# Performance work log

Hardware: AMD Instinct MI355X
Metric: run time of the kernel (lower is better)

Reference implementation:

```python
import jax, jax.numpy as jnp
import numpy as np
from jax import lax

N_NODES = 50000
N_EDGES = 1_600_000
B, T = 4, 12
GCN_H, TCN_H, OUT_LEN = 32, 32, 1


def setup_inputs() -> dict:
    key = jax.random.key(0)
    ks = jax.random.split(key, 8)
    return {
        "x_seq": jax.random.normal(ks[0], (B, T, N_NODES), jnp.float32),
        "edge_index": jax.random.randint(ks[1], (2, N_EDGES), 0, N_NODES, jnp.int64),
        "edge_weight": jax.random.uniform(ks[2], (N_EDGES,), jnp.float32),
        "gcn_w": jax.random.normal(ks[3], (1, GCN_H), jnp.float32) * 0.5,
        "gcn_b": jnp.zeros((GCN_H,), jnp.float32),
        "conv_w": jax.random.normal(ks[4], (TCN_H, GCN_H, 3), jnp.float32) * 0.1,
        "conv_b": jnp.zeros((TCN_H,), jnp.float32),
        "lin_w": jax.random.normal(ks[5], (TCN_H, OUT_LEN), jnp.float32) * 0.1,
        "lin_b": jnp.zeros((OUT_LEN,), jnp.float32),
    }


def _gcn_agg(x, src, dst, norm, n):
    msgs = x[:, src] * norm[None, :]                      # [BT, E+N]
    return jax.vmap(lambda m: jax.ops.segment_sum(m, dst, num_segments=n))(msgs)


def reference(x_seq, edge_index, edge_weight, gcn_w, gcn_b, conv_w, conv_b, lin_w, lin_b):
    b, t, n = x_seq.shape
    src, dst = edge_index[0], edge_index[1]
    # GCN normalization with self-loops (fill_value=1.0), as PyG GCNConv
    loops = jnp.arange(n)
    src_f = jnp.concatenate([src, loops])
    dst_f = jnp.concatenate([dst, loops])
    ew_f = jnp.concatenate([edge_weight, jnp.ones((n,), x_seq.dtype)])
    deg = jax.ops.segment_sum(ew_f, dst_f, num_segments=n)
    dinv = jnp.where(deg > 0, deg ** -0.5, 0.0)
    norm = dinv[src_f] * ew_f * dinv[dst_f]               # [E+N]
    # GCN is linear: A_hat (X W) == (A_hat X) W ; X has 1 channel -> aggregate scalars
    x = x_seq.reshape(b * t, n)                           # [BT, N]
    agg = _gcn_agg(x, src_f, dst_f, norm, n)              # [BT, N]
    h = agg[..., None] * gcn_w[0][None, None, :] + gcn_b  # [BT, N, H]
    # temporal conv over T: reshape to [B*N, H, T]
    h = h.reshape(b, t, n, GCN_H).transpose(0, 2, 3, 1).reshape(b * n, GCN_H, t)
    y = lax.conv_general_dilated(h, conv_w, window_strides=(1,), padding=[(1, 1)],
                                 dimension_numbers=("NCH", "OIH", "NCH"))
    y = jax.nn.relu(y + conv_b[None, :, None])            # [B*N, H, T]
    pooled = y.mean(axis=-1)                              # [B*N, H]
    out = pooled @ lin_w + lin_b                          # [B*N, out_len]
    return out.reshape(b, n, -1).transpose(0, 2, 1)       # [B, out_len, N]
```

## Files before the change

kernel.cpp:

```cpp
#include <hip/hip_runtime.h>
#include <hip/hip_fp16.h>
#include <math.h>

#define N_NODES 50000
#define N_EDGES 1600000
#define BT 48
#define CAP 80
#define BINSZ 64
#define NBINS 782
#define ECHUNK 4096
#define SBLOCK 1024

__global__ __launch_bounds__(SBLOCK) void stage_k(const int* __restrict__ ei,
                                                  const float* __restrict__ ew,
                                                  int* __restrict__ stage_cnt,
                                                  int2* __restrict__ staged,
                                                  int scap) {
  __shared__ int hist[NBINS];
  __shared__ int ptr[NBINS];
  int t = threadIdx.x;
  for (int b = t; b < NBINS; b += SBLOCK) hist[b] = 0;
  __syncthreads();

  int e0 = blockIdx.x * ECHUNK;
  int ne = min(ECHUNK, N_EDGES - e0);

  for (int k = t; k < ne; k += SBLOCK) {
    int d = ei[N_EDGES + e0 + k];
    atomicAdd(&hist[d >> 6], 1);
  }
  __syncthreads();
  for (int b = t; b < NBINS; b += SBLOCK) {
    int h = hist[b];
    ptr[b] = h ? atomicAdd(&stage_cnt[b], h) : 0;
  }
  __syncthreads();
  for (int k = t; k < ne; k += SBLOCK) {
    int e = e0 + k;
    int s = ei[e];
    int d = ei[N_EDGES + e];
    float w = ew[e];
    int b = d >> 6;
    int p = atomicAdd(&ptr[b], 1);
    if (p < scap)
      staged[(size_t)b * scap + p] = make_int2(s | ((d & 63) << 16), __float_as_int(w));
  }
}

__global__ __launch_bounds__(256) void build_k(const int2* __restrict__ staged,
                                               const int* __restrict__ stage_cnt,
                                               int2* __restrict__ ell,
                                               int* __restrict__ cnt,
                                               float* __restrict__ dinv,
                                               int scap) {
  __shared__ int2 rows[BINSZ][CAP];
  __shared__ int rcnt[BINSZ];
  int t = threadIdx.x, b = blockIdx.x;
  if (t < BINSZ) rcnt[t] = 0;
  __syncthreads();

  int ne = min(stage_cnt[b], scap);
  const int2* sp = staged + (size_t)b * scap;
  for (int k = t; k < ne; k += 256) {
    int2 m = sp[k];
    int dloc = (m.x >> 16) & 63;
    int src  = m.x & 0xffff;
    int slot = atomicAdd(&rcnt[dloc], 1);
    if (slot < CAP) rows[dloc][slot] = make_int2(src, m.y);
  }
  __syncthreads();

  int base = b * BINSZ;
  if (t < BINSZ) {
    int n = base + t;
    if (n < N_NODES) {
      int c = min(rcnt[t], CAP);
      float s = 0.0f;
      for (int i = 0; i < c; ++i) s += __int_as_float(rows[t][i].y);
      cnt[n] = c;
      dinv[n] = 1.0f / sqrtf(1.0f + s);
    }
  }
  __syncthreads();

  int r = t & 63, st = t >> 6;
  int n = base + r;
  if (n < N_NODES) {
    int c = min(rcnt[r], CAP);
    int2* dst = ell + (size_t)n * CAP;
    for (int i = st; i < c; i += 4) dst[i] = rows[r][i];
  }
}

__global__ __launch_bounds__(256) void transpose_k(const float* __restrict__ x,
                                                   const float* __restrict__ dinv,
                                                   __half* __restrict__ xs) {
  int n = blockIdx.x * 256 + threadIdx.x;
  if (n >= N_NODES) return;
  float dn = dinv[n];
  __half2 h2[BT / 2];
#pragma unroll
  for (int j = 0; j < BT / 2; ++j) {
    float a = dn * x[(size_t)(2 * j) * N_NODES + n];
    float b = dn * x[(size_t)(2 * j + 1) * N_NODES + n];
    h2[j] = __floats2half2_rn(a, b);
  }
  float4* dst = (float4*)(xs + (size_t)n * BT);
  const float4* srcp = (const float4*)h2;
#pragma unroll
  for (int j = 0; j < 6; ++j) dst[j] = srcp[j];
}

__global__ void coeff_k(const float* __restrict__ conv_w, const float* __restrict__ gcn_w,
                        const float* __restrict__ gcn_b, float* __restrict__ wv,
                        float* __restrict__ wb) {
  int idx = threadIdx.x;
  if (idx >= 96) return;
  int co = idx / 3, k = idx % 3;
  float sv = 0.0f, sb = 0.0f;
  for (int ci = 0; ci < 32; ++ci) {
    float w = conv_w[co * 96 + ci * 3 + k];
    sv += w * gcn_w[ci];
    sb += w * gcn_b[ci];
  }
  wv[idx] = sv;
  wb[idx] = sb;
}

__global__ __launch_bounds__(256) void spmm_epi_k(const __half* __restrict__ xs,
                                                  const int2* __restrict__ ell,
                                                  const int* __restrict__ cnt,
                                                  const float* __restrict__ dinv,
                                                  const float* __restrict__ wv,
                                                  const float* __restrict__ wb,
                                                  const float* __restrict__ conv_b,
                                                  const float* __restrict__ lin_w,
                                                  const float* __restrict__ lin_b,
                                                  float* __restrict__ out) {
  __shared__ float s_wv[96], s_wb[96], s_cb[32], s_lw[32];
  __shared__ float s_lb;
  __shared__ float sAgg[4][BT];
  int tid = threadIdx.x;
  if (tid < 96) { s_wv[tid] = wv[tid]; s_wb[tid] = wb[tid]; }
  if (tid < 32) { s_cb[tid] = conv_b[tid]; s_lw[tid] = lin_w[tid]; }
  if (tid == 0) s_lb = lin_b[0];
  __syncthreads();

  int lane = tid & 63;
  int wid  = tid >> 6;
  int n = (blockIdx.x * 256 + tid) >> 6;
  int col = (lane < BT) ? lane : (BT - 1);
  const int2* pp = ell + (size_t)n * CAP;
  int c = __builtin_amdgcn_readfirstlane(cnt[n]);
  int2 m = pp[lane];
  float acc = 0.0f;
  int cm = (c < 64) ? c : 64;

  int e = 0;
  for (; e + 16 <= cm; e += 16) {
    float xv[16], wgt[16];
#pragma unroll
    for (int k = 0; k < 16; ++k) {
      int s  = __builtin_amdgcn_readlane(m.x, e + k);
      wgt[k] = __int_as_float(__builtin_amdgcn_readlane(m.y, e + k));
      xv[k]  = __half2float(xs[(size_t)s * BT + col]);
    }
#pragma unroll
    for (int k = 0; k < 16; ++k) acc = fmaf(wgt[k], xv[k], acc);
  }
  for (; e + 8 <= cm; e += 8) {
    float xv[8], wgt[8];
#pragma unroll
    for (int k = 0; k < 8; ++k) {
      int s  = __builtin_amdgcn_readlane(m.x, e + k);
      wgt[k] = __int_as_float(__builtin_amdgcn_readlane(m.y, e + k));
      xv[k]  = __half2float(xs[(size_t)s * BT + col]);
    }
#pragma unroll
    for (int k = 0; k < 8; ++k) acc = fmaf(wgt[k], xv[k], acc);
  }
  for (; e < cm; ++e) {
    int   s = __builtin_amdgcn_readlane(m.x, e);
    float w = __int_as_float(__builtin_amdgcn_readlane(m.y, e));
    acc = fmaf(w, __half2float(xs[(size_t)s * BT + col]), acc);
  }
  for (; e < c; ++e) {
    int2 q = pp[e];
    int   s = __builtin_amdgcn_readfirstlane(q.x);
    float w = __int_as_float(__builtin_amdgcn_readfirstlane(q.y));
    acc = fmaf(w, __half2float(xs[(size_t)s * BT + col]), acc);
  }

  float dn = dinv[n];
  float xsn = __half2float(xs[(size_t)n * BT + col]);
  if (lane < BT) sAgg[wid][col] = dn * (acc + xsn);

  int b = lane >> 4;
  float a[14];
  a[0] = 0.0f; a[13] = 0.0f;
#pragma unroll
  for (int t = 0; t < 12; ++t) a[t + 1] = sAgg[wid][b * 12 + t];

  float part = 0.0f;
#pragma unroll
  for (int cc = 0; cc < 2; ++cc) {
    int co = (lane & 15) + cc * 16;
    float w0 = s_wv[3 * co], w1 = s_wv[3 * co + 1], w2 = s_wv[3 * co + 2];
    float b0 = s_wb[3 * co], b1 = s_wb[3 * co + 1], b2 = s_wb[3 * co + 2];
    float base = s_cb[co] + b1;
    float lw = s_lw[co];
    float sr = 0.0f;
#pragma unroll
    for (int t = 0; t < 12; ++t) {
      float v = base + w0 * a[t] + w1 * a[t + 1] + w2 * a[t + 2];
      if (t > 0)  v += b0;
      if (t < 11) v += b2;
      sr += fmaxf(v, 0.0f);
    }
    part = fmaf(lw, sr, part);
  }
  part += __shfl_xor(part, 1, 64);
  part += __shfl_xor(part, 2, 64);
  part += __shfl_xor(part, 4, 64);
  part += __shfl_xor(part, 8, 64);
  if ((lane & 15) == 0)
    out[(size_t)b * N_NODES + n] = s_lb + part * (1.0f / 12.0f);
}

extern "C" void kernel_launch(void* const* d_in, const int* in_sizes, int n_in,
                              void* d_out, int out_size, void* d_ws, size_t ws_size,
                              hipStream_t stream) {
  const float* x_seq  = (const float*)d_in[0];
  const int*   ei     = (const int*)d_in[1];
  const float* ew     = (const float*)d_in[2];
  const float* gcn_w  = (const float*)d_in[3];
  const float* gcn_b  = (const float*)d_in[4];
  const float* conv_w = (const float*)d_in[5];
  const float* conv_b = (const float*)d_in[6];
  const float* lin_w  = (const float*)d_in[7];
  const float* lin_b  = (const float*)d_in[8];
  float* out = (float*)d_out;

  char* ws = (char*)d_ws;
  size_t off = 0;
  auto alloc = [&](size_t bytes) -> void* {
    void* p = ws + off;
    off += (bytes + 511) & ~(size_t)511;
    return p;
  };
  float* dinv = (float*)alloc((size_t)N_NODES * 4);
  int*   cnt  = (int*)alloc((size_t)N_NODES * 4);
  float* wv   = (float*)alloc(96 * 4);
  float* wb   = (float*)alloc(96 * 4);
  int*   sc   = (int*)alloc((size_t)NBINS * 4);
  int2*  ell  = (int2*)alloc((size_t)N_NODES * CAP * 8);

  size_t remain = (ws_size > off) ? (ws_size - off) : 0;
  int scap = (int)(remain / ((size_t)NBINS * 8));
  if (scap > 4096) scap = 4096;
  if (scap < 3072) scap = 3072;
  int2* staged = (int2*)alloc((size_t)NBINS * scap * 8);
  __half* xs = (__half*)staged;

  const int nblk = (N_NODES + 255) / 256;
  const int sblk = (N_EDGES + ECHUNK - 1) / ECHUNK;
  const int wblk = (N_NODES * 64) / 256;

  hipMemsetAsync(sc, 0, (size_t)NBINS * 4, stream);
  hipLaunchKernelGGL(stage_k, dim3(sblk), dim3(SBLOCK), 0, stream, ei, ew, sc, staged, scap);
  hipLaunchKernelGGL(build_k, dim3(NBINS), dim3(256), 0, stream, staged, sc, ell, cnt, dinv, scap);
  hipLaunchKernelGGL(transpose_k, dim3(nblk), dim3(256), 0, stream, x_seq, dinv, xs);
  hipLaunchKernelGGL(coeff_k, dim3(1), dim3(128), 0, stream, conv_w, gcn_w, gcn_b, wv, wb);
  hipLaunchKernelGGL(spmm_epi_k, dim3(wblk), dim3(256), 0, stream,
                     xs, ell, cnt, dinv, wv, wb, conv_b, lin_w, lin_b, out);
}
```

Baseline: 188.7 us.

## Replace padded ELL with compact CSR packing 16-bit src and fp16 weight

Replaces the fixed-capacity ELL (80 int2 slots per node) with a compact CSR-like array. A new single-block scan kernel computes per-bin base offsets, and each row gets a descriptor holding its start offset and count. Each edge is packed into one 32-bit word: a 16-bit source index and an fp16 weight. This cuts edge-list write and read traffic by more than half, at the cost of an extra launch, a serial per-bin prefix in build_k, and reduced weight precision.

```diff
diff --git a/kernel.cpp b/kernel.cpp
--- a/kernel.cpp
+++ b/kernel.cpp
@@ -47,14 +47,32 @@
   }
 }
 
+__global__ __launch_bounds__(1024) void scan_k(const int* __restrict__ sc,
+                                               int* __restrict__ bin_base) {
+  __shared__ int buf[1024];
+  int t = threadIdx.x;
+  int v = (t < NBINS) ? sc[t] : 0;
+  buf[t] = v;
+  __syncthreads();
+  for (int off = 1; off < 1024; off <<= 1) {
+    int x = (t >= off) ? buf[t - off] : 0;
+    __syncthreads();
+    buf[t] += x;
+    __syncthreads();
+  }
+  if (t < NBINS) bin_base[t] = buf[t] - v;
+}
+
 __global__ __launch_bounds__(256) void build_k(const int2* __restrict__ staged,
                                                const int* __restrict__ stage_cnt,
-                                               int2* __restrict__ ell,
-                                               int* __restrict__ cnt,
+                                               const int* __restrict__ bin_base,
+                                               int* __restrict__ packed,
+                                               int* __restrict__ row_desc,
                                                float* __restrict__ dinv,
                                                int scap) {
   __shared__ int2 rows[BINSZ][CAP];
   __shared__ int rcnt[BINSZ];
+  __shared__ int loc[BINSZ + 1];
   int t = threadIdx.x, b = blockIdx.x;
   if (t < BINSZ) rcnt[t] = 0;
   __syncthreads();
@@ -70,15 +88,26 @@
   }
   __syncthreads();
 
+  if (t == 0) {
+    int run = 0;
+    for (int r = 0; r < BINSZ; ++r) {
+      loc[r] = run;
+      run += min(rcnt[r], CAP);
+    }
+    loc[BINSZ] = run;
+  }
+  __syncthreads();
+
   int base = b * BINSZ;
+  int gbase = bin_base[b];
   if (t < BINSZ) {
     int n = base + t;
     if (n < N_NODES) {
       int c = min(rcnt[t], CAP);
       float s = 0.0f;
       for (int i = 0; i < c; ++i) s += __int_as_float(rows[t][i].y);
-      cnt[n] = c;
       dinv[n] = 1.0f / sqrtf(1.0f + s);
+      row_desc[n] = ((gbase + loc[t]) << 7) | c;
     }
   }
   __syncthreads();
@@ -87,8 +116,12 @@
   int n = base + r;
   if (n < N_NODES) {
     int c = min(rcnt[r], CAP);
-    int2* dst = ell + (size_t)n * CAP;
-    for (int i = st; i < c; i += 4) dst[i] = rows[r][i];
+    int* dst = packed + gbase + loc[r];
+    for (int i = st; i < c; i += 4) {
+      int2 e = rows[r][i];
+      unsigned hw = __half_as_ushort(__float2half_rn(__int_as_float(e.y)));
+      dst[i] = (e.x & 0xffff) | ((int)hw << 16);
+    }
   }
 }
 
@@ -128,8 +161,8 @@
 }
 
 __global__ __launch_bounds__(256) void spmm_epi_k(const __half* __restrict__ xs,
-                                                  const int2* __restrict__ ell,
-                                                  const int* __restrict__ cnt,
+                                                  const int* __restrict__ packed,
+                                                  const int* __restrict__ row_desc,
                                                   const float* __restrict__ dinv,
                                                   const float* __restrict__ wv,
                                                   const float* __restrict__ wb,
@@ -150,49 +183,54 @@
   int wid  = tid >> 6;
   int n = (blockIdx.x * 256 + tid) >> 6;
   int col = (lane < BT) ? lane : (BT - 1);
-  const int2* pp = ell + (size_t)n * CAP;
-  int c = __builtin_amdgcn_readfirstlane(cnt[n]);
-  int2 m = pp[lane];
+  int desc = __builtin_amdgcn_readfirstlane(row_desc[n]);
+  int c     = desc & 127;
+  int start = ((unsigned)desc) >> 7;
+  const int* pp = packed + start;
+  int m = pp[lane];
   float acc = 0.0f;
   int cm = (c < 64) ? c : 64;
 
   int e = 0;
   for (; e + 16 <= cm; e += 16) {
-    float xv[16], wgt[16];
+    float xv[16], wg[16];
 #pragma unroll
     for (int k = 0; k < 16; ++k) {
-      int s  = __builtin_amdgcn_readlane(m.x, e + k);
-      wgt[k] = __int_as_float(__builtin_amdgcn_readlane(m.y, e + k));
-      xv[k]  = __half2float(xs[(size_t)s * BT + col]);
-    }
-#pragma unroll
-    for (int k = 0; k < 16; ++k) acc = fmaf(wgt[k], xv[k], acc);
+      int u = __builtin_amdgcn_readlane(m, e + k);
+      int s = u & 0xffff;
+      wg[k] = __half2float(__ushort_as_half((unsigned short)(((unsigned)u) >> 16)));
+      xv[k] = __half2float(xs[s * BT + col]);
+    }
+#pragma unroll
+    for (int k = 0; k < 16; ++k) acc = fmaf(wg[k], xv[k], acc);
   }
   for (; e + 8 <= cm; e += 8) {
-    float xv[8], wgt[8];
+    float xv[8], wg[8];
 #pragma unroll
     for (int k = 0; k < 8; ++k) {
-      int s  = __builtin_amdgcn_readlane(m.x, e + k);
-      wgt[k] = __int_as_float(__builtin_amdgcn_readlane(m.y, e + k));
-      xv[k]  = __half2float(xs[(size_t)s * BT + col]);
-    }
-#pragma unroll
-    for (int k = 0; k < 8; ++k) acc = fmaf(wgt[k], xv[k], acc);
+      int u = __builtin_amdgcn_readlane(m, e + k);
+      int s = u & 0xffff;
+      wg[k] = __half2float(__ushort_as_half((unsigned short)(((unsigned)u) >> 16)));
+      xv[k] = __half2float(xs[s * BT + col]);
+    }
+#pragma unroll
+    for (int k = 0; k < 8; ++k) acc = fmaf(wg[k], xv[k], acc);
   }
   for (; e < cm; ++e) {
-    int   s = __builtin_amdgcn_readlane(m.x, e);
-    float w = __int_as_float(__builtin_amdgcn_readlane(m.y, e));
-    acc = fmaf(w, __half2float(xs[(size_t)s * BT + col]), acc);
+    int u = __builtin_amdgcn_readlane(m, e);
+    int s = u & 0xffff;
+    float w = __half2float(__ushort_as_half((unsigned short)(((unsigned)u) >> 16)));
+    acc = fmaf(w, __half2float(xs[s * BT + col]), acc);
   }
   for (; e < c; ++e) {
-    int2 q = pp[e];
-    int   s = __builtin_amdgcn_readfirstlane(q.x);
-    float w = __int_as_float(__builtin_amdgcn_readfirstlane(q.y));
-    acc = fmaf(w, __half2float(xs[(size_t)s * BT + col]), acc);
+    int u = __builtin_amdgcn_readfirstlane(pp[e]);
+    int s = u & 0xffff;
+    float w = __half2float(__ushort_as_half((unsigned short)(((unsigned)u) >> 16)));
+    acc = fmaf(w, __half2float(xs[s * BT + col]), acc);
   }
 
   float dn = dinv[n];
-  float xsn = __half2float(xs[(size_t)n * BT + col]);
+  float xsn = __half2float(xs[n * BT + col]);
   if (lane < BT) sAgg[wid][col] = dn * (acc + xsn);
 
   int b = lane >> 4;
@@ -248,12 +286,13 @@
     off += (bytes + 511) & ~(size_t)511;
     return p;
   };
-  float* dinv = (float*)alloc((size_t)N_NODES * 4);
-  int*   cnt  = (int*)alloc((size_t)N_NODES * 4);
-  float* wv   = (float*)alloc(96 * 4);
-  float* wb   = (float*)alloc(96 * 4);
-  int*   sc   = (int*)alloc((size_t)NBINS * 4);
-  int2*  ell  = (int2*)alloc((size_t)N_NODES * CAP * 8);
+  float* dinv    = (float*)alloc((size_t)N_NODES * 4);
+  int*   rdesc   = (int*)alloc((size_t)N_NODES * 4);
+  float* wv      = (float*)alloc(96 * 4);
+  float* wb      = (float*)alloc(96 * 4);
+  int*   sc      = (int*)alloc((size_t)NBINS * 4);
+  int*   bbase   = (int*)alloc((size_t)NBINS * 4);
+  int*   packed  = (int*)alloc(((size_t)N_EDGES + 64) * 4);
 
   size_t remain = (ws_size > off) ? (ws_size - off) : 0;
   int scap = (int)(remain / ((size_t)NBINS * 8));
@@ -268,9 +307,11 @@
 
   hipMemsetAsync(sc, 0, (size_t)NBINS * 4, stream);
   hipLaunchKernelGGL(stage_k, dim3(sblk), dim3(SBLOCK), 0, stream, ei, ew, sc, staged, scap);
-  hipLaunchKernelGGL(build_k, dim3(NBINS), dim3(256), 0, stream, staged, sc, ell, cnt, dinv, scap);
+  hipLaunchKernelGGL(scan_k, dim3(1), dim3(1024), 0, stream, sc, bbase);
+  hipLaunchKernelGGL(build_k, dim3(NBINS), dim3(256), 0, stream,
+                     staged, sc, bbase, packed, rdesc, dinv, scap);
   hipLaunchKernelGGL(transpose_k, dim3(nblk), dim3(256), 0, stream, x_seq, dinv, xs);
   hipLaunchKernelGGL(coeff_k, dim3(1), dim3(128), 0, stream, conv_w, gcn_w, gcn_b, wv, wb);
   hipLaunchKernelGGL(spmm_epi_k, dim3(wblk), dim3(256), 0, stream,
-                     xs, ell, cnt, dinv, wv, wb, conv_b, lin_w, lin_b, out);
-}
+                     xs, packed, rdesc, dinv, wv, wb, conv_b, lin_w, lin_b, out);
+}
```

New measurement: 190.4 us. No clear change (+0.9%).
